# Kernel optimization log

Measured on AMD Instinct MI355X. Metric: run time of the kernel, lower is better.

## Reference

```python
import jax, jax.numpy as jnp
import numpy as np

INPUTSIZE = 1024
OUTPUTSIZE = 1024
FEATUREMAPS = 16
BITS = (INPUTSIZE - 1).bit_length()  # 10
BATCH = 2048


def _make_fm():
    # fm[k, j, i] = (i ^ (1 << j)) % inputsize  (same for every feature map k)
    i = np.arange(OUTPUTSIZE, dtype=np.int64)
    j = (1 << np.arange(BITS, dtype=np.int64))[:, None]
    fm_bits_out = (i[None, :] ^ j) % INPUTSIZE  # [bits, out]
    fm = np.broadcast_to(fm_bits_out[None], (FEATUREMAPS, BITS, OUTPUTSIZE)).copy()
    return jnp.asarray(fm, dtype=jnp.int32)


def setup_inputs() -> dict:
    key = jax.random.key(0)
    k1, k2, k3 = jax.random.split(key, 3)
    std = 0.5 / BITS
    x = jax.random.normal(k1, (BATCH, INPUTSIZE), dtype=jnp.float32)
    weights = jax.random.normal(k2, (FEATUREMAPS, BITS, OUTPUTSIZE), dtype=jnp.float32) * std
    bias = jax.random.normal(k3, (FEATUREMAPS, OUTPUTSIZE), dtype=jnp.float32) * std
    return {"x": x, "weights": weights, "bias": bias, "fm": _make_fm()}


def _resize(t, newsize):
    # Static-shape version of Layer.resize (column crop/tile)
    cur = t.shape[1]
    if newsize < cur:
        return t[:, :newsize]
    if newsize > cur:
        mult = (newsize + cur - 1) // cur
        return jnp.tile(t, (1, mult))[:, :newsize]
    return t


def reference(x, weights, bias, fm):
    # gather: [B, F, bits, O]
    gathered = x[:, fm]
    # multiply by weights [F, bits, O] and reduce over bits -> [B, F, O]
    net = jnp.einsum('bfjo,fjo->bfo', gathered, weights) + bias
    flat = net.reshape(x.shape[0], FEATUREMAPS * OUTPUTSIZE)
    tiled = jnp.tile(_resize(x, OUTPUTSIZE), (1, FEATUREMAPS))
    return flat + tiled
```

## Files before the change

### kernel.cpp

```cpp
#include <hip/hip_runtime.h>


#define BTILE 16
#define NSLOT 5

__global__ __launch_bounds__(128, 2) void hypercube_kernel(
    const float* __restrict__ x,
    const float* __restrict__ w,
    const float* __restrict__ bias,
    float* __restrict__ out)
{
    __shared__ float xs[BTILE * NSLOT * 64];

    const int tid   = threadIdx.x;
    const int lane  = tid & 63;
    const int wave  = tid >> 6;

    const int bid   = blockIdx.x;
    const int xcd   = bid & 7;
    const int ix    = bid >> 3;
    const int btile = xcd * 16 + (ix >> 4);
    const int chunk = ix & 15;

    const int b0    = btile * BTILE;
    const int f0    = wave * 8;
    const int o     = chunk * 64 + lane;

    #pragma unroll
    for (int it = 0; it < (BTILE * NSLOT * 64 / 4) / 128; ++it) {
        const int q    = it * 128 + tid;
        const int row  = q / (NSLOT * 16);
        const int rem  = q - row * (NSLOT * 16);
        const int slot = rem >> 4;
        const int l4   = (rem & 15) << 2;
        const int src_chunk = chunk ^ ((1 << slot) >> 1);
        const float4 v = *(const float4*)&x[(size_t)(b0 + row) * 1024 + src_chunk * 64 + l4];
        *(float4*)&xs[q * 4] = v;
    }

    float wr[8][10], br[8];
    #pragma unroll
    for (int ff = 0; ff < 8; ++ff) {
        const int f = f0 + ff;
        #pragma unroll
        for (int j = 0; j < 10; ++j)
            wr[ff][j] = w[(f * 10 + j) * 1024 + o];
        br[ff] = bias[f * 1024 + o];
    }

    __syncthreads();

    #pragma unroll 2
    for (int row = 0; row < BTILE; ++row) {
        const float* __restrict__ xr = &xs[row * (NSLOT * 64)];
        const float x0 = xr[lane];
        const float g0 = xr[lane ^ 1];
        const float g1 = xr[lane ^ 2];
        const float g2 = xr[lane ^ 4];
        const float g3 = xr[lane ^ 8];
        const float g4 = xr[lane ^ 16];
        const float g5 = xr[lane ^ 32];
        const float g6 = xr[64  + lane];
        const float g7 = xr[128 + lane];
        const float g8 = xr[192 + lane];
        const float g9 = xr[256 + lane];

        float* __restrict__ ob = out + (size_t)(b0 + row) * 16384 + chunk * 64 + lane;
        #pragma unroll
        for (int ff = 0; ff < 8; ++ff) {
            float acc = br[ff] + x0;
            acc = fmaf(g0, wr[ff][0], acc);
            acc = fmaf(g1, wr[ff][1], acc);
            acc = fmaf(g2, wr[ff][2], acc);
            acc = fmaf(g3, wr[ff][3], acc);
            acc = fmaf(g4, wr[ff][4], acc);
            acc = fmaf(g5, wr[ff][5], acc);
            acc = fmaf(g6, wr[ff][6], acc);
            acc = fmaf(g7, wr[ff][7], acc);
            acc = fmaf(g8, wr[ff][8], acc);
            acc = fmaf(g9, wr[ff][9], acc);
            __builtin_nontemporal_store(acc, &ob[(f0 + ff) * 1024]);
        }
    }
}

extern "C" void kernel_launch(void* const* d_in, const int* in_sizes, int n_in,
                              void* d_out, int out_size, void* d_ws, size_t ws_size,
                              hipStream_t stream) {
    const float* x    = (const float*)d_in[0];
    const float* w    = (const float*)d_in[1];
    const float* bias = (const float*)d_in[2];
    float* out = (float*)d_out;

    dim3 grid(16 * (2048 / BTILE));
    dim3 block(128);
    hypercube_kernel<<<grid, block, 0, stream>>>(x, w, bias, out);
}
```

Before: 155.6 us.

## Vectorize hypercube kernel to float4 per lane with 256-wide output chunks

Each lane now computes four consecutive outputs, using float4 loads for x, weights and bias, and float4 nontemporal stores. Each block covers 256 outputs × 8 features × 8 batch rows with 256 threads, and stages three 256-wide x slots in shared memory; the two lowest hypercube bits come from inside the register vector. This cuts LDS and global instruction counts and widens stores, at the cost of more weight registers per thread and a smaller batch tile, which means less weight reuse per block.

```diff
diff --git a/kernel.cpp b/kernel.cpp
--- a/kernel.cpp
+++ b/kernel.cpp
@@ -1,85 +1,89 @@
 #include <hip/hip_runtime.h>
 
 
-#define BTILE 16
-#define NSLOT 5
+#define BTILE 8
 
-__global__ __launch_bounds__(128, 2) void hypercube_kernel(
+typedef float fx4 __attribute__((ext_vector_type(4)));
+
+__global__ __launch_bounds__(256, 3) void hypercube_kernel(
     const float* __restrict__ x,
     const float* __restrict__ w,
     const float* __restrict__ bias,
     float* __restrict__ out)
 {
-    __shared__ float xs[BTILE * NSLOT * 64];
+    __shared__ float xs[BTILE * 3 * 256];
 
-    const int tid   = threadIdx.x;
-    const int lane  = tid & 63;
-    const int wave  = tid >> 6;
+    const int tid  = threadIdx.x;
+    const int lane = tid & 63;
+    const int wave = tid >> 6;
 
     const int bid   = blockIdx.x;
     const int xcd   = bid & 7;
     const int ix    = bid >> 3;
-    const int btile = xcd * 16 + (ix >> 4);
-    const int chunk = ix & 15;
+    const int btile = xcd * 32 + (ix >> 3);
+    const int sub   = ix & 7;
+    const int oc    = sub >> 1;
+    const int fblk  = sub & 1;
 
     const int b0    = btile * BTILE;
-    const int f0    = wave * 8;
-    const int o     = chunk * 64 + lane;
+    const int obase = oc * 256;
 
     #pragma unroll
-    for (int it = 0; it < (BTILE * NSLOT * 64 / 4) / 128; ++it) {
-        const int q    = it * 128 + tid;
-        const int row  = q / (NSLOT * 16);
-        const int rem  = q - row * (NSLOT * 16);
-        const int slot = rem >> 4;
-        const int l4   = (rem & 15) << 2;
-        const int src_chunk = chunk ^ ((1 << slot) >> 1);
-        const float4 v = *(const float4*)&x[(size_t)(b0 + row) * 1024 + src_chunk * 64 + l4];
-        *(float4*)&xs[q * 4] = v;
+    for (int it = 0; it < 6; ++it) {
+        const int q    = it * 256 + tid;
+        const int row  = q / 192;
+        const int rem  = q - row * 192;
+        const int slot = rem >> 6;
+        const int col  = (rem & 63) << 2;
+        const fx4 v = *(const fx4*)&x[(size_t)(b0 + row) * 1024 + (oc ^ slot) * 256 + col];
+        *(fx4*)&xs[q * 4] = v;
     }
 
-    float wr[8][10], br[8];
+    const int fw0 = fblk * 8 + wave * 2;
+    float wr[2][10][4], br[2][4];
     #pragma unroll
-    for (int ff = 0; ff < 8; ++ff) {
-        const int f = f0 + ff;
+    for (int ff = 0; ff < 2; ++ff) {
         #pragma unroll
         for (int j = 0; j < 10; ++j)
-            wr[ff][j] = w[(f * 10 + j) * 1024 + o];
-        br[ff] = bias[f * 1024 + o];
+            *(fx4*)wr[ff][j] = *(const fx4*)&w[(size_t)((fw0 + ff) * 10 + j) * 1024 + obase + lane * 4];
+        *(fx4*)br[ff] = *(const fx4*)&bias[(size_t)(fw0 + ff) * 1024 + obase + lane * 4];
     }
 
     __syncthreads();
 
-    #pragma unroll 2
     for (int row = 0; row < BTILE; ++row) {
-        const float* __restrict__ xr = &xs[row * (NSLOT * 64)];
-        const float x0 = xr[lane];
-        const float g0 = xr[lane ^ 1];
-        const float g1 = xr[lane ^ 2];
-        const float g2 = xr[lane ^ 4];
-        const float g3 = xr[lane ^ 8];
-        const float g4 = xr[lane ^ 16];
-        const float g5 = xr[lane ^ 32];
-        const float g6 = xr[64  + lane];
-        const float g7 = xr[128 + lane];
-        const float g8 = xr[192 + lane];
-        const float g9 = xr[256 + lane];
+        const float* __restrict__ xr = &xs[row * 768];
+        float v0[4], v4[4], v8[4], v16[4], v32[4], v64[4], v128[4], v256[4], v512[4];
+        *(fx4*)v0   = *(const fx4*)&xr[lane * 4];
+        *(fx4*)v4   = *(const fx4*)&xr[(lane ^ 1)  * 4];
+        *(fx4*)v8   = *(const fx4*)&xr[(lane ^ 2)  * 4];
+        *(fx4*)v16  = *(const fx4*)&xr[(lane ^ 4)  * 4];
+        *(fx4*)v32  = *(const fx4*)&xr[(lane ^ 8)  * 4];
+        *(fx4*)v64  = *(const fx4*)&xr[(lane ^ 16) * 4];
+        *(fx4*)v128 = *(const fx4*)&xr[(lane ^ 32) * 4];
+        *(fx4*)v256 = *(const fx4*)&xr[256 + lane * 4];
+        *(fx4*)v512 = *(const fx4*)&xr[512 + lane * 4];
 
-        float* __restrict__ ob = out + (size_t)(b0 + row) * 16384 + chunk * 64 + lane;
+        float* __restrict__ ob = out + (size_t)(b0 + row) * 16384 + obase + lane * 4;
         #pragma unroll
-        for (int ff = 0; ff < 8; ++ff) {
-            float acc = br[ff] + x0;
-            acc = fmaf(g0, wr[ff][0], acc);
-            acc = fmaf(g1, wr[ff][1], acc);
-            acc = fmaf(g2, wr[ff][2], acc);
-            acc = fmaf(g3, wr[ff][3], acc);
-            acc = fmaf(g4, wr[ff][4], acc);
-            acc = fmaf(g5, wr[ff][5], acc);
-            acc = fmaf(g6, wr[ff][6], acc);
-            acc = fmaf(g7, wr[ff][7], acc);
-            acc = fmaf(g8, wr[ff][8], acc);
-            acc = fmaf(g9, wr[ff][9], acc);
-            __builtin_nontemporal_store(acc, &ob[(f0 + ff) * 1024]);
+        for (int ff = 0; ff < 2; ++ff) {
+            fx4 av;
+            #pragma unroll
+            for (int k = 0; k < 4; ++k) {
+                float a = br[ff][k] + v0[k];
+                a = fmaf(v0[k ^ 1], wr[ff][0][k], a);
+                a = fmaf(v0[k ^ 2], wr[ff][1][k], a);
+                a = fmaf(v4[k],     wr[ff][2][k], a);
+                a = fmaf(v8[k],     wr[ff][3][k], a);
+                a = fmaf(v16[k],    wr[ff][4][k], a);
+                a = fmaf(v32[k],    wr[ff][5][k], a);
+                a = fmaf(v64[k],    wr[ff][6][k], a);
+                a = fmaf(v128[k],   wr[ff][7][k], a);
+                a = fmaf(v256[k],   wr[ff][8][k], a);
+                a = fmaf(v512[k],   wr[ff][9][k], a);
+                av[k] = a;
+            }
+            __builtin_nontemporal_store(av, (fx4*)&ob[(fw0 + ff) * 1024]);
         }
     }
 }
@@ -92,7 +96,7 @@
     const float* bias = (const float*)d_in[2];
     float* out = (float*)d_out;
 
-    dim3 grid(16 * (2048 / BTILE));
-    dim3 block(128);
+    dim3 grid(2048);
+    dim3 block(256);
     hypercube_kernel<<<grid, block, 0, stream>>>(x, w, bias, out);
 }
```

Result: no change. 156.2 us (+0.4%).
